# Performance work log

Hardware: AMD Instinct MI355X
Metric: run time of the kernel (lower is better)

## Reference

```python
import jax, jax.numpy as jnp
import numpy as np

B, S, D = 4, 2048, 1024  # batch, seq_len, input_dim (= dk = dv)


def setup_inputs() -> dict:
    key = jax.random.key(0)
    kx, kq, kk, kv = jax.random.split(key, 4)
    scale = 1.0 / np.sqrt(D)
    return {
        "x": jax.random.normal(kx, (B, S, D), dtype=jnp.float32),
        "Wq": jax.random.normal(kq, (D, D), dtype=jnp.float32) * scale,
        "Wk": jax.random.normal(kk, (D, D), dtype=jnp.float32) * scale,
        "Wv": jax.random.normal(kv, (D, D), dtype=jnp.float32) * scale,
    }


def reference(x, Wq, Wk, Wv):
    # Linear projections (bias=False). W is [in, out].
    Q = jnp.einsum("bsd,de->bse", x, Wq)
    K = jnp.einsum("bsd,de->bse", x, Wk)
    V = jnp.einsum("bsd,de->bse", x, Wv)
    dk = Q.shape[-1]
    # scores: [B, S, S]
    scores = jnp.einsum("bqe,bke->bqk", Q, K) / jnp.sqrt(jnp.float32(dk))
    # causal mask: upper triangle (j > i) masked to -inf
    S_len = x.shape[1]
    causal = jnp.triu(jnp.ones((S_len, S_len), dtype=bool), k=1)
    scores = jnp.where(causal[None, :, :], -jnp.inf, scores)
    attn = jax.nn.softmax(scores, axis=-1)
    # dropout p=0.0 (eval): identity
    return jnp.einsum("bqk,bke->bqe", attn, V)
```

## Files before the change

kernel.cpp:

```cpp
#include <hip/hip_runtime.h>

#define S_LEN 2048
#define DMODEL 1024
#define NBATCH 4

typedef unsigned short u16;
typedef __bf16 bf16x8 __attribute__((ext_vector_type(8)));
typedef float f32x4 __attribute__((ext_vector_type(4)));

typedef __attribute__((address_space(3))) unsigned lds_u32;
typedef const __attribute__((address_space(1))) unsigned glb_u32;

__device__ __forceinline__ u16 f2bf(float f) {
  union { float f; unsigned u; } v;
  v.f = f;
  unsigned r = v.u + 0x7fffu + ((v.u >> 16) & 1u);
  return (u16)(r >> 16);
}

__device__ __forceinline__ float bf2f(u16 h) {
  union { unsigned u; float f; } v;
  v.u = ((unsigned)h) << 16;
  return v.f;
}

__global__ void convert_x_kernel(const float* __restrict__ x, u16* __restrict__ xb, long n) {
  long i = ((long)blockIdx.x * blockDim.x + threadIdx.x) * 4;
  long stride = (long)gridDim.x * blockDim.x * 4;
  for (; i < n; i += stride) {
    float4 v = *reinterpret_cast<const float4*>(x + i);
    ushort4 o;
    o.x = f2bf(v.x); o.y = f2bf(v.y); o.z = f2bf(v.z); o.w = f2bf(v.w);
    *reinterpret_cast<ushort4*>(xb + i) = o;
  }
}

__global__ void transpose_w_kernel(const float* __restrict__ W, u16* __restrict__ Wt) {
  __shared__ float tile[32][33];
  int tx = threadIdx.x, ty = threadIdx.y;
  int k0 = blockIdx.x * 32, n0 = blockIdx.y * 32;
#pragma unroll
  for (int i = 0; i < 32; i += 8)
    tile[ty + i][tx] = W[(long)(k0 + ty + i) * DMODEL + n0 + tx];
  __syncthreads();
#pragma unroll
  for (int i = 0; i < 32; i += 8)
    Wt[(long)(n0 + ty + i) * DMODEL + k0 + tx] = f2bf(tile[tx][ty + i]);
}


#define STG(SRCP, LD, ISB, H, T, BUFB) do { \
    const u16* _s = (SRCP) + (long)(H) * 128 * (LD) + (T) * 64; \
    char* _d = lds + (BUFB) * 65536 + ((ISB) ? 32768 : 0) + ((H) * 8 + w) * 2048; \
    __builtin_amdgcn_global_load_lds((glb_u32*)_s, (lds_u32*)_d, 16, 0, 0); \
    __builtin_amdgcn_global_load_lds((glb_u32*)(_s + 32), (lds_u32*)(_d + 1024), 16, 0, 0); \
  } while (0)

#define READ_B() do { \
    _Pragma("unroll") \
    for (int _q = 0; _q < 2; ++_q) \
      _Pragma("unroll") \
      for (int _j = 0; _j < 2; ++_j) { \
        int _np = _q * 8 + wn * 2 + _j; \
        bfr[_q][_j][0] = *(const bf16x8*)(_Bl + (_np * 2 + 0) * 1024 + frag_off); \
        bfr[_q][_j][1] = *(const bf16x8*)(_Bl + (_np * 2 + 1) * 1024 + frag_off); \
      } \
  } while (0)

#define READ_A(QM) do { \
    _Pragma("unroll") \
    for (int _i = 0; _i < 4; ++_i) { \
      int _mp = (QM) * 8 + wm * 4 + _i; \
      af[_i][0] = *(const bf16x8*)(_Al + (_mp * 2 + 0) * 1024 + frag_off); \
      af[_i][1] = *(const bf16x8*)(_Al + (_mp * 2 + 1) * 1024 + frag_off); \
    } \
  } while (0)

#define MFMA32(QM) do { \
    _Pragma("unroll") \
    for (int _i = 0; _i < 4; ++_i) \
      _Pragma("unroll") \
      for (int _q = 0; _q < 2; ++_q) \
        _Pragma("unroll") \
        for (int _j = 0; _j < 2; ++_j) { \
          acc[QM][_q][_i][_j] = __builtin_amdgcn_mfma_f32_16x16x32_bf16(af[_i][0], bfr[_q][_j][0], acc[QM][_q][_i][_j], 0, 0, 0); \
          acc[QM][_q][_i][_j] = __builtin_amdgcn_mfma_f32_16x16x32_bf16(af[_i][1], bfr[_q][_j][1], acc[QM][_q][_i][_j], 0, 0, 0); \
        } \
  } while (0)

template<int CMODE, int CAUSAL>
__global__ __launch_bounds__(512, 2) void gemm256(
    const u16* __restrict__ A, const u16* __restrict__ B, void* __restrict__ Cptr,
    int lda, int ldb, int ldc, int Kdim,
    long sAz, long sBz, long sCz)
{
  int bm = blockIdx.x, bn = blockIdx.y, bz = blockIdx.z;
  if (CAUSAL == 1 && bn > bm) return;
  int Keff = Kdim;
  if (CAUSAL == 2) { int lim = (bm + 1) * 256; if (lim < Keff) Keff = lim; }
  int NT = Keff >> 6;

  const u16* Ab = A + (long)bz * sAz + (long)bm * 256 * lda;
  const u16* Bb = B + (long)bz * sBz + (long)bn * 256 * ldb;

  __shared__ char lds[131072];

  int tid = threadIdx.x;
  int lane = tid & 63, w = tid >> 6;
  int wm = w >> 2, wn = w & 3;
  int l15 = lane & 15, lhi = lane >> 4;
  int frag_off = (l15 * 64 + lhi * 16) ^ (((lane >> 3) & 1) << 5);

  int le = lane ^ ((lane >> 5) << 1);
  int lr = le >> 2;
  int kb = (le & 3) * 8;

  const u16* Asrc = Ab + (long)(w * 16 + lr) * lda + kb;
  const u16* Bsrc = Bb + (long)(w * 16 + lr) * ldb + kb;

  f32x4 acc[2][2][4][2];
#pragma unroll
  for (int a = 0; a < 2; ++a)
#pragma unroll
    for (int b = 0; b < 2; ++b)
#pragma unroll
      for (int c = 0; c < 4; ++c)
#pragma unroll
        for (int d = 0; d < 2; ++d)
          acc[a][b][c][d] = (f32x4){0.f, 0.f, 0.f, 0.f};

  STG(Asrc, lda, 0, 0, 0, 0); STG(Bsrc, ldb, 1, 0, 0, 0);
  STG(Asrc, lda, 0, 1, 0, 0); STG(Bsrc, ldb, 1, 1, 0, 0);
  STG(Asrc, lda, 0, 0, 1, 1); STG(Bsrc, ldb, 1, 0, 1, 1);
  asm volatile("s_waitcnt vmcnt(4)" ::: "memory");
  __builtin_amdgcn_s_barrier();

  for (int g = 0; g < NT; ++g) {
    int buf = g & 1;
    int t1 = g + 1; if (t1 >= NT) t1 -= NT;
    int t2 = g + 2; if (t2 >= NT) t2 -= NT;
    const char* _Al = lds + buf * 65536;
    const char* _Bl = _Al + 32768;
    bf16x8 af[4][2], bfr[2][2][2];

    READ_B();
    READ_A(0);
    STG(Asrc, lda, 0, 1, t1, buf ^ 1);
    STG(Bsrc, ldb, 1, 1, t1, buf ^ 1);
    __builtin_amdgcn_s_barrier();
    asm volatile("s_waitcnt lgkmcnt(0)" ::: "memory");
    __builtin_amdgcn_sched_barrier(0);
    __builtin_amdgcn_s_setprio(1);
    MFMA32(0);
    __builtin_amdgcn_s_setprio(0);
    __builtin_amdgcn_s_barrier();

    READ_A(1);
    STG(Asrc, lda, 0, 0, t2, buf);
    STG(Bsrc, ldb, 1, 0, t2, buf);
    __builtin_amdgcn_s_barrier();
    asm volatile("s_waitcnt lgkmcnt(0)" ::: "memory");
    __builtin_amdgcn_sched_barrier(0);
    __builtin_amdgcn_s_setprio(1);
    MFMA32(1);
    __builtin_amdgcn_s_setprio(0);
    asm volatile("s_waitcnt vmcnt(4)" ::: "memory");
    __builtin_amdgcn_s_barrier();
  }

  int Mbase = bm * 256, Nbase = bn * 256;
#pragma unroll
  for (int qm = 0; qm < 2; ++qm)
#pragma unroll
    for (int qn = 0; qn < 2; ++qn)
#pragma unroll
      for (int i = 0; i < 4; ++i)
#pragma unroll
        for (int j = 0; j < 2; ++j) {
          int r0 = Mbase + qm * 128 + wm * 64 + i * 16 + lhi * 4;
          int col = Nbase + qn * 128 + wn * 32 + j * 16 + l15;
          f32x4 v = acc[qm][qn][i][j];
          if constexpr (CMODE == 0) {
            float* C = (float*)Cptr + (long)bz * sCz;
#pragma unroll
            for (int r = 0; r < 4; ++r)
              C[(long)(r0 + r) * ldc + col] = v[r];
          } else if constexpr (CMODE == 1) {
            u16* C = (u16*)Cptr + (long)bz * sCz;
#pragma unroll
            for (int r = 0; r < 4; ++r)
              C[(long)(r0 + r) * ldc + col] = f2bf(v[r]);
          } else {
            if (col < 2048) {
              u16* dst = (u16*)Cptr + (col >= 1024 ? 8388608 : 0);
              int c = col & 1023;
#pragma unroll
              for (int r = 0; r < 4; ++r)
                dst[(long)(r0 + r) * 1024 + c] = f2bf(v[r]);
            } else {
              u16* Vt = (u16*)Cptr + 16777216;
              int e = col - 2048;
              int bb = r0 >> 11, s = r0 & 2047;
              ushort4 u;
              u.x = f2bf(v[0]); u.y = f2bf(v[1]); u.z = f2bf(v[2]); u.w = f2bf(v[3]);
              *reinterpret_cast<ushort4*>(Vt + ((long)bb * 1024 + e) * 2048 + s) = u;
            }
          }
        }
}

__global__ __launch_bounds__(256) void softmax1p(const u16* __restrict__ sc,
                                                 u16* __restrict__ P) {
  int q = blockIdx.x, b = blockIdx.y;
  const u16* srow = sc + ((long)b * S_LEN + q) * S_LEN;
  u16* prow = P + ((long)b * S_LEN + q) * S_LEN;
  int n = q + 1;
  int nz = ((q >> 8) + 1) << 8;
  int tid = threadIdx.x;
  int j0 = tid * 8;
  const float scale = 0.03125f;

  __shared__ float red[8];

  float vs[8];
#pragma unroll
  for (int e = 0; e < 8; ++e) vs[e] = -1e30f;
  if (j0 < n) {
    ushort4 a = *reinterpret_cast<const ushort4*>(srow + j0);
    ushort4 c = *reinterpret_cast<const ushort4*>(srow + j0 + 4);
    vs[0] = bf2f(a.x) * scale; vs[1] = bf2f(a.y) * scale;
    vs[2] = bf2f(a.z) * scale; vs[3] = bf2f(a.w) * scale;
    vs[4] = bf2f(c.x) * scale; vs[5] = bf2f(c.y) * scale;
    vs[6] = bf2f(c.z) * scale; vs[7] = bf2f(c.w) * scale;
#pragma unroll
    for (int e = 0; e < 8; ++e)
      if (j0 + e >= n) vs[e] = -1e30f;
  }

  float m = -1e30f;
#pragma unroll
  for (int e = 0; e < 8; ++e) m = fmaxf(m, vs[e]);
#pragma unroll
  for (int off = 32; off > 0; off >>= 1) m = fmaxf(m, __shfl_xor(m, off, 64));
  if ((tid & 63) == 0) red[tid >> 6] = m;
  __syncthreads();
  float ms = fmaxf(fmaxf(red[0], red[1]), fmaxf(red[2], red[3]));

  float p[8];
  float s = 0.f;
#pragma unroll
  for (int e = 0; e < 8; ++e) { p[e] = __expf(vs[e] - ms); s += (j0 + e < n) ? p[e] : 0.f; }
#pragma unroll
  for (int off = 32; off > 0; off >>= 1) s += __shfl_xor(s, off, 64);
  __syncthreads();
  if ((tid & 63) == 0) red[4 + (tid >> 6)] = s;
  __syncthreads();
  float inv = 1.f / (red[4] + red[5] + red[6] + red[7]);

  if (j0 < nz) {
    ushort4 o0, o1;
    o0.x = (j0 + 0 < n) ? f2bf(p[0] * inv) : (u16)0;
    o0.y = (j0 + 1 < n) ? f2bf(p[1] * inv) : (u16)0;
    o0.z = (j0 + 2 < n) ? f2bf(p[2] * inv) : (u16)0;
    o0.w = (j0 + 3 < n) ? f2bf(p[3] * inv) : (u16)0;
    o1.x = (j0 + 4 < n) ? f2bf(p[4] * inv) : (u16)0;
    o1.y = (j0 + 5 < n) ? f2bf(p[5] * inv) : (u16)0;
    o1.z = (j0 + 6 < n) ? f2bf(p[6] * inv) : (u16)0;
    o1.w = (j0 + 7 < n) ? f2bf(p[7] * inv) : (u16)0;
    *reinterpret_cast<ushort4*>(prow + j0) = o0;
    *reinterpret_cast<ushort4*>(prow + j0 + 4) = o1;
  }
}

extern "C" void kernel_launch(void* const* d_in, const int* in_sizes, int n_in,
                              void* d_out, int out_size, void* d_ws, size_t ws_size,
                              hipStream_t stream) {
  const float* x  = (const float*)d_in[0];
  const float* Wq = (const float*)d_in[1];
  const float* Wk = (const float*)d_in[2];
  const float* Wv = (const float*)d_in[3];
  float* out = (float*)d_out;

  char* ws = (char*)d_ws;
  u16* xb  = (u16*)(ws);
  u16* wtb = (u16*)(ws + 16777216);
  u16* Qb  = (u16*)(ws + 23068672);
  u16* Kb  = (u16*)(ws + 39845888);
  u16* Vtb = (u16*)(ws + 56623104);
  u16* scb = (u16*)(ws + 73400320);
  u16* P   = (u16*)(ws + 106954752);

  long nx = (long)NBATCH * S_LEN * DMODEL;
  convert_x_kernel<<<2048, 256, 0, stream>>>(x, xb, nx);

  dim3 tb(32, 8);
  transpose_w_kernel<<<dim3(32, 32), tb, 0, stream>>>(Wq, wtb);
  transpose_w_kernel<<<dim3(32, 32), tb, 0, stream>>>(Wk, wtb + 1024 * 1024);
  transpose_w_kernel<<<dim3(32, 32), tb, 0, stream>>>(Wv, wtb + 2 * 1024 * 1024);

  gemm256<3, 0><<<dim3(32, 12, 1), 512, 0, stream>>>(
      xb, wtb, Qb, DMODEL, DMODEL, 0, DMODEL, 0, 0, 0);

  gemm256<1, 1><<<dim3(8, 8, 4), 512, 0, stream>>>(
      Qb, Kb, scb, DMODEL, DMODEL, S_LEN, DMODEL,
      (long)S_LEN * DMODEL, (long)S_LEN * DMODEL, (long)S_LEN * S_LEN);

  softmax1p<<<dim3(S_LEN, NBATCH), 256, 0, stream>>>(scb, P);

  gemm256<0, 2><<<dim3(8, 4, 4), 512, 0, stream>>>(
      P, Vtb, out, S_LEN, S_LEN, DMODEL, S_LEN,
      (long)S_LEN * S_LEN, (long)DMODEL * S_LEN, (long)S_LEN * DMODEL);
}
```

Baseline: 185.8 us.

## Split GEMM main loop into four quadrant phases interleaving loads with MFMA

The 256x256 GEMM main loop now runs four quarter-sized MFMA phases instead of two half phases. B fragments are read per N-quadrant and kept in two register sets, and each A/B global-to-LDS stage is issued in its own phase. The aim is to spread global load issue and LDS reads more evenly across compute, and to lower peak register use for B fragments. In exchange it adds more barriers per iteration, and the reordered buffer writes must still respect which LDS halves are already consumed.

```diff
diff --git a/kernel.cpp b/kernel.cpp
--- a/kernel.cpp
+++ b/kernel.cpp
@@ -56,17 +56,6 @@
     __builtin_amdgcn_global_load_lds((glb_u32*)(_s + 32), (lds_u32*)(_d + 1024), 16, 0, 0); \
   } while (0)
 
-#define READ_B() do { \
-    _Pragma("unroll") \
-    for (int _q = 0; _q < 2; ++_q) \
-      _Pragma("unroll") \
-      for (int _j = 0; _j < 2; ++_j) { \
-        int _np = _q * 8 + wn * 2 + _j; \
-        bfr[_q][_j][0] = *(const bf16x8*)(_Bl + (_np * 2 + 0) * 1024 + frag_off); \
-        bfr[_q][_j][1] = *(const bf16x8*)(_Bl + (_np * 2 + 1) * 1024 + frag_off); \
-      } \
-  } while (0)
-
 #define READ_A(QM) do { \
     _Pragma("unroll") \
     for (int _i = 0; _i < 4; ++_i) { \
@@ -76,16 +65,23 @@
     } \
   } while (0)
 
-#define MFMA32(QM) do { \
+#define READ_BQ(DST, QN) do { \
+    _Pragma("unroll") \
+    for (int _j = 0; _j < 2; ++_j) { \
+      int _np = (QN) * 8 + wn * 2 + _j; \
+      DST[_j][0] = *(const bf16x8*)(_Bl + (_np * 2 + 0) * 1024 + frag_off); \
+      DST[_j][1] = *(const bf16x8*)(_Bl + (_np * 2 + 1) * 1024 + frag_off); \
+    } \
+  } while (0)
+
+#define MFMA16(QM, QN, BREG) do { \
     _Pragma("unroll") \
     for (int _i = 0; _i < 4; ++_i) \
       _Pragma("unroll") \
-      for (int _q = 0; _q < 2; ++_q) \
-        _Pragma("unroll") \
-        for (int _j = 0; _j < 2; ++_j) { \
-          acc[QM][_q][_i][_j] = __builtin_amdgcn_mfma_f32_16x16x32_bf16(af[_i][0], bfr[_q][_j][0], acc[QM][_q][_i][_j], 0, 0, 0); \
-          acc[QM][_q][_i][_j] = __builtin_amdgcn_mfma_f32_16x16x32_bf16(af[_i][1], bfr[_q][_j][1], acc[QM][_q][_i][_j], 0, 0, 0); \
-        } \
+      for (int _j = 0; _j < 2; ++_j) { \
+        acc[QM][QN][_i][_j] = __builtin_amdgcn_mfma_f32_16x16x32_bf16(af[_i][0], BREG[_j][0], acc[QM][QN][_i][_j], 0, 0, 0); \
+        acc[QM][QN][_i][_j] = __builtin_amdgcn_mfma_f32_16x16x32_bf16(af[_i][1], BREG[_j][1], acc[QM][QN][_i][_j], 0, 0, 0); \
+      } \
   } while (0)
 
 template<int CMODE, int CAUSAL>
@@ -141,28 +137,43 @@
     int t2 = g + 2; if (t2 >= NT) t2 -= NT;
     const char* _Al = lds + buf * 65536;
     const char* _Bl = _Al + 32768;
-    bf16x8 af[4][2], bfr[2][2][2];
-
-    READ_B();
+    bf16x8 af[4][2], b0[2][2], b1[2][2];
+
     READ_A(0);
+    READ_BQ(b0, 0);
     STG(Asrc, lda, 0, 1, t1, buf ^ 1);
-    STG(Bsrc, ldb, 1, 1, t1, buf ^ 1);
     __builtin_amdgcn_s_barrier();
     asm volatile("s_waitcnt lgkmcnt(0)" ::: "memory");
     __builtin_amdgcn_sched_barrier(0);
     __builtin_amdgcn_s_setprio(1);
-    MFMA32(0);
+    MFMA16(0, 0, b0);
     __builtin_amdgcn_s_setprio(0);
     __builtin_amdgcn_s_barrier();
 
-    READ_A(1);
-    STG(Asrc, lda, 0, 0, t2, buf);
-    STG(Bsrc, ldb, 1, 0, t2, buf);
+    READ_BQ(b1, 1);
+    STG(Bsrc, ldb, 1, 1, t1, buf ^ 1);
     __builtin_amdgcn_s_barrier();
     asm volatile("s_waitcnt lgkmcnt(0)" ::: "memory");
     __builtin_amdgcn_sched_barrier(0);
     __builtin_amdgcn_s_setprio(1);
-    MFMA32(1);
+    MFMA16(0, 1, b1);
+    __builtin_amdgcn_s_setprio(0);
+    __builtin_amdgcn_s_barrier();
+
+    READ_A(1);
+    STG(Asrc, lda, 0, 0, t2, buf);
+    __builtin_amdgcn_s_barrier();
+    asm volatile("s_waitcnt lgkmcnt(0)" ::: "memory");
+    __builtin_amdgcn_sched_barrier(0);
+    __builtin_amdgcn_s_setprio(1);
+    MFMA16(1, 1, b1);
+    __builtin_amdgcn_s_setprio(0);
+    __builtin_amdgcn_s_barrier();
+
+    STG(Bsrc, ldb, 1, 0, t2, buf);
+    __builtin_amdgcn_s_barrier();
+    __builtin_amdgcn_s_setprio(1);
+    MFMA16(1, 0, b0);
     __builtin_amdgcn_s_setprio(0);
     asm volatile("s_waitcnt vmcnt(4)" ::: "memory");
     __builtin_amdgcn_s_barrier();
```

New measurement: 185.7 us. Within noise of the previous version (-0.1%).
